# Performance work log

Measured on AMD Instinct MI355X. Metric: run time of the kernel, lower is better.

Reference implementation:

```python
import jax, jax.numpy as jnp
import numpy as np

B, S, D = 512, 512, 768
VOCAB = 30522
CLS, SEP, PAD = 101, 102, 0


def setup_inputs() -> dict:
    key = jax.random.key(0)
    k1, k2 = jax.random.split(key)
    embed = jax.random.normal(k1, (B, S, D), dtype=jnp.float32)
    token_ids = jax.random.randint(k2, (B, S), 0, VOCAB, dtype=jnp.int64)
    return {"embed": embed, "token_ids": token_ids}


def reference(embed, token_ids):
    # mask out [CLS]=101, [SEP]=102, [PAD]=0; mean over remaining tokens
    mask = (token_ids != CLS) & (token_ids != SEP) & (token_ids != PAD)  # [B, S]
    maskf = mask.astype(embed.dtype)
    summed = jnp.einsum('bsd,bs->bd', embed, maskf)           # [B, D]
    count = jnp.sum(maskf, axis=-1, keepdims=True)            # [B, 1]
    return summed / count
```

## Files before the change

### kernel.cpp

```cpp
#include <hip/hip_runtime.h>


constexpr int B  = 512;
constexpr int S  = 512;
constexpr int D  = 768;
constexpr int NV = D / 4;
constexpr int CH = 4;
constexpr int SCH = S / CH;
constexpr int NT = NV * CH;

__global__ __launch_bounds__(NT) void masked_mean_kernel(
    const float4* __restrict__ embed,
    const int* __restrict__ tok,
    float4* __restrict__ out)
{
    const int b = blockIdx.x;
    const int t = threadIdx.x;

    const int w    = t >> 6;
    const int lane = t & 63;
    const int col  = (w % 3) * 64 + lane;
    const int ch   = w / 3;

    __shared__ float  maskf[S];
    __shared__ float4 accs[CH][NV];
    __shared__ float  cnts[CH];

    if (t < S) {
        const int id = tok[b * S + t];
        maskf[t] = (id != 0 && id != 101 && id != 102) ? 1.0f : 0.0f;
    }
    __syncthreads();

    const int s0 = ch * SCH;
    const float4* row = embed + (size_t)b * S * NV + (size_t)s0 * NV + col;
    float4 acc = make_float4(0.f, 0.f, 0.f, 0.f);
    float cnt = 0.f;

#pragma unroll 8
    for (int s = 0; s < SCH; ++s) {
        const float  m = maskf[s0 + s];
        const float4 v = row[(size_t)s * NV];
        cnt += m;
        acc.x = fmaf(v.x, m, acc.x);
        acc.y = fmaf(v.y, m, acc.y);
        acc.z = fmaf(v.z, m, acc.z);
        acc.w = fmaf(v.w, m, acc.w);
    }

    accs[ch][col] = acc;
    if (col == 0) cnts[ch] = cnt;
    __syncthreads();

    if (t < NV) {
        float4 a = accs[0][t];
#pragma unroll
        for (int k = 1; k < CH; ++k) {
            const float4 p = accs[k][t];
            a.x += p.x; a.y += p.y; a.z += p.z; a.w += p.w;
        }
        const float c = cnts[0] + cnts[1] + cnts[2] + cnts[3];
        const float inv = 1.0f / c;
        out[b * NV + t] = make_float4(a.x * inv, a.y * inv, a.z * inv, a.w * inv);
    }
}

extern "C" void kernel_launch(void* const* d_in, const int* in_sizes, int n_in,
                              void* d_out, int out_size, void* d_ws, size_t ws_size,
                              hipStream_t stream) {
    const float4* embed = (const float4*)d_in[0];
    const int* tok = (const int*)d_in[1];
    float4* out = (float4*)d_out;

    masked_mean_kernel<<<dim3(B), dim3(NT), 0, stream>>>(embed, tok, out);
}
```

Baseline: 991.4 us.

## Split sequence reduction across four blocks per batch with finalize kernel

The single block per batch row is replaced by four blocks, each reducing a quarter of the sequence into a workspace. A second kernel then sums the four partials and divides by the count. Each thread now handles three float4 columns, which raises memory-level parallelism per thread, and the grid has 2048 smaller blocks instead of 512 large ones for better occupancy and load balance. The cost is an extra launch plus a workspace write and read of the partials.

After: 998.6 us. No clear change (+0.7%).

```diff
diff --git a/kernel.cpp b/kernel.cpp
--- a/kernel.cpp
+++ b/kernel.cpp
@@ -5,64 +5,97 @@
 constexpr int S  = 512;
 constexpr int D  = 768;
 constexpr int NV = D / 4;
-constexpr int CH = 4;
-constexpr int SCH = S / CH;
-constexpr int NT = NV * CH;
+constexpr int P  = 4;
+constexpr int SP = S / P;
+constexpr int WAVES = 4;
+constexpr int RW = SP / WAVES;
 
-__global__ __launch_bounds__(NT) void masked_mean_kernel(
+__global__ __launch_bounds__(256) void partial_kernel(
     const float4* __restrict__ embed,
-    const int* __restrict__ tok,
-    float4* __restrict__ out)
+    const int*    __restrict__ tok,
+    float4*       __restrict__ ws_sum,
+    float*        __restrict__ ws_cnt)
+{
+    const int bp   = blockIdx.x;
+    const int b    = bp >> 2;
+    const int p    = bp & (P - 1);
+    const int t    = threadIdx.x;
+    const int w    = t >> 6;
+    const int lane = t & 63;
+
+    __shared__ float  maskf[SP];
+    __shared__ float4 sacc[WAVES][NV];
+    __shared__ float  scnt[WAVES];
+
+    const int sbase = p * SP;
+
+    if (t < SP) {
+        const int id = tok[b * S + sbase + t];
+        maskf[t] = (id != 0 && id != 101 && id != 102) ? 1.0f : 0.0f;
+    }
+    __syncthreads();
+
+    const int r0 = w * RW;
+    const float4* rowp = embed + ((size_t)b * S + sbase + r0) * NV + lane;
+
+    float4 a0 = make_float4(0.f, 0.f, 0.f, 0.f);
+    float4 a1 = make_float4(0.f, 0.f, 0.f, 0.f);
+    float4 a2 = make_float4(0.f, 0.f, 0.f, 0.f);
+    float  cnt = 0.f;
+
+#pragma unroll 2
+    for (int r = 0; r < RW; ++r) {
+        const float  m  = maskf[r0 + r];
+        const float4 v0 = rowp[(size_t)r * NV];
+        const float4 v1 = rowp[(size_t)r * NV + 64];
+        const float4 v2 = rowp[(size_t)r * NV + 128];
+        cnt += m;
+        a0.x = fmaf(v0.x, m, a0.x); a0.y = fmaf(v0.y, m, a0.y);
+        a0.z = fmaf(v0.z, m, a0.z); a0.w = fmaf(v0.w, m, a0.w);
+        a1.x = fmaf(v1.x, m, a1.x); a1.y = fmaf(v1.y, m, a1.y);
+        a1.z = fmaf(v1.z, m, a1.z); a1.w = fmaf(v1.w, m, a1.w);
+        a2.x = fmaf(v2.x, m, a2.x); a2.y = fmaf(v2.y, m, a2.y);
+        a2.z = fmaf(v2.z, m, a2.z); a2.w = fmaf(v2.w, m, a2.w);
+    }
+
+    sacc[w][lane]       = a0;
+    sacc[w][lane + 64]  = a1;
+    sacc[w][lane + 128] = a2;
+    if (lane == 0) scnt[w] = cnt;
+    __syncthreads();
+
+    if (t < NV) {
+        float4 s0 = sacc[0][t];
+        const float4 s1 = sacc[1][t];
+        const float4 s2 = sacc[2][t];
+        const float4 s3 = sacc[3][t];
+        s0.x += s1.x + s2.x + s3.x;
+        s0.y += s1.y + s2.y + s3.y;
+        s0.z += s1.z + s2.z + s3.z;
+        s0.w += s1.w + s2.w + s3.w;
+        ws_sum[(size_t)bp * NV + t] = s0;
+    }
+    if (t == 0) ws_cnt[bp] = scnt[0] + scnt[1] + scnt[2] + scnt[3];
+}
+
+__global__ __launch_bounds__(NV) void finalize_kernel(
+    const float4* __restrict__ ws_sum,
+    const float*  __restrict__ ws_cnt,
+    float4*       __restrict__ out)
 {
     const int b = blockIdx.x;
     const int t = threadIdx.x;
 
-    const int w    = t >> 6;
-    const int lane = t & 63;
-    const int col  = (w % 3) * 64 + lane;
-    const int ch   = w / 3;
-
-    __shared__ float  maskf[S];
-    __shared__ float4 accs[CH][NV];
-    __shared__ float  cnts[CH];
-
-    if (t < S) {
-        const int id = tok[b * S + t];
-        maskf[t] = (id != 0 && id != 101 && id != 102) ? 1.0f : 0.0f;
+    float4 a = make_float4(0.f, 0.f, 0.f, 0.f);
+#pragma unroll
+    for (int p = 0; p < P; ++p) {
+        const float4 v = ws_sum[((size_t)(b * P + p)) * NV + t];
+        a.x += v.x; a.y += v.y; a.z += v.z; a.w += v.w;
     }
-    __syncthreads();
-
-    const int s0 = ch * SCH;
-    const float4* row = embed + (size_t)b * S * NV + (size_t)s0 * NV + col;
-    float4 acc = make_float4(0.f, 0.f, 0.f, 0.f);
-    float cnt = 0.f;
-
-#pragma unroll 8
-    for (int s = 0; s < SCH; ++s) {
-        const float  m = maskf[s0 + s];
-        const float4 v = row[(size_t)s * NV];
-        cnt += m;
-        acc.x = fmaf(v.x, m, acc.x);
-        acc.y = fmaf(v.y, m, acc.y);
-        acc.z = fmaf(v.z, m, acc.z);
-        acc.w = fmaf(v.w, m, acc.w);
-    }
-
-    accs[ch][col] = acc;
-    if (col == 0) cnts[ch] = cnt;
-    __syncthreads();
-
-    if (t < NV) {
-        float4 a = accs[0][t];
-#pragma unroll
-        for (int k = 1; k < CH; ++k) {
-            const float4 p = accs[k][t];
-            a.x += p.x; a.y += p.y; a.z += p.z; a.w += p.w;
-        }
-        const float c = cnts[0] + cnts[1] + cnts[2] + cnts[3];
-        const float inv = 1.0f / c;
-        out[b * NV + t] = make_float4(a.x * inv, a.y * inv, a.z * inv, a.w * inv);
-    }
+    const float c = ws_cnt[b * P + 0] + ws_cnt[b * P + 1]
+                  + ws_cnt[b * P + 2] + ws_cnt[b * P + 3];
+    const float inv = 1.0f / c;
+    out[b * NV + t] = make_float4(a.x * inv, a.y * inv, a.z * inv, a.w * inv);
 }
 
 extern "C" void kernel_launch(void* const* d_in, const int* in_sizes, int n_in,
@@ -72,5 +105,9 @@
     const int* tok = (const int*)d_in[1];
     float4* out = (float4*)d_out;
 
-    masked_mean_kernel<<<dim3(B), dim3(NT), 0, stream>>>(embed, tok, out);
+    float4* ws_sum = (float4*)d_ws;
+    float*  ws_cnt = (float*)((char*)d_ws + (size_t)B * P * NV * sizeof(float4));
+
+    partial_kernel<<<dim3(B * P), dim3(256), 0, stream>>>(embed, tok, ws_sum, ws_cnt);
+    finalize_kernel<<<dim3(B), dim3(NV), 0, stream>>>(ws_sum, ws_cnt, out);
 }
```
